# Kernel optimization log

Hardware: AMD Instinct MI355X
Metric: run time of the kernel (lower is better)

## Reference

```python
import jax, jax.numpy as jnp
import numpy as np

B, NUM, LENTH, AUX = 32, 64, 64, 64
SIZE, OUT = 256, 256
IN_G = (LENTH + 1) * 2 + AUX  # 194


def _linear_params(k, fan_in, fan_out):
    # torch nn.Linear default init: U(-1/sqrt(fan_in), 1/sqrt(fan_in))
    s = 1.0 / np.sqrt(fan_in)
    kw, kb = jax.random.split(k)
    W = jax.random.uniform(kw, (fan_in, fan_out), minval=-s, maxval=s, dtype=jnp.float32)
    b = jax.random.uniform(kb, (fan_out,), minval=-s, maxval=s, dtype=jnp.float32)
    return W, b


def setup_inputs() -> dict:
    key = jax.random.key(0)
    ks = jax.random.split(key, 8)
    inp = {"x_aux": jax.random.normal(ks[0], (B, NUM, LENTH + AUX), dtype=jnp.float32)}
    dims = [("g1", IN_G, SIZE), ("g2", SIZE, SIZE), ("g3", SIZE, SIZE), ("g4", SIZE, OUT),
            ("f1", OUT, SIZE), ("f2", SIZE, SIZE), ("f3", SIZE, OUT)]
    for k, (name, fi, fo) in zip(ks[1:], dims):
        W, b = _linear_params(k, fi, fo)
        inp[name + "_w"] = W
        inp[name + "_b"] = b
    return inp


def reference(x_aux, g1_w, g1_b, g2_w, g2_b, g3_w, g3_b, g4_w, g4_b,
              f1_w, f1_b, f2_w, f2_b, f3_w, f3_b):
    bsz = x_aux.shape[0]
    # coord feature = object index i
    coord = jnp.broadcast_to(
        jnp.arange(NUM, dtype=x_aux.dtype)[None, :, None], (bsz, NUM, 1))
    x = jnp.concatenate([x_aux[:, :, :LENTH], coord], axis=-1)      # [B, N, LENTH+1]
    xa = jnp.concatenate([x_aux, coord], axis=-1)                   # [B, N, LENTH+AUX+1]
    # all-pairs broadcast+concat -> [B, N, N, IN_G]
    x_i = jnp.broadcast_to(x[:, None, :, :], (bsz, NUM, NUM, LENTH + 1))
    x_j = jnp.broadcast_to(xa[:, :, None, :], (bsz, NUM, NUM, LENTH + AUX + 1))
    pairs = jnp.concatenate([x_i, x_j], axis=-1)
    # shared g-MLP over every pair
    h = jax.nn.relu(pairs @ g1_w + g1_b)
    h = jax.nn.relu(h @ g2_w + g2_b)
    h = jax.nn.relu(h @ g3_w + g3_b)
    h = jax.nn.relu(h @ g4_w + g4_b)
    # sum-pool over all N*N pairs -> [B, OUT]
    x_g = h.sum(axis=(1, 2))
    # f-MLP (dropout treated as identity / eval mode)
    x_f = jax.nn.relu(x_g @ f1_w + f1_b)
    x_f = jax.nn.relu(x_f @ f2_w + f2_b)
    return x_f @ f3_w + f3_b
```

## Files before the change

### kernel.cpp

```cpp
#include <hip/hip_runtime.h>

#define BATCH 32
#define NOBJ  64
#define PADK  264

typedef _Float16 f16x2 __attribute__((ext_vector_type(2)));
typedef _Float16 f16x4 __attribute__((ext_vector_type(4)));
typedef _Float16 f16x8 __attribute__((ext_vector_type(8)));
typedef float    f32x4 __attribute__((ext_vector_type(4)));
typedef float    f32x16 __attribute__((ext_vector_type(16)));

#define MFMA32(a, b, c) __builtin_amdgcn_mfma_f32_32x32x16_f16((a), (b), (c), 0, 0, 0)


__global__ __launch_bounds__(256) void prep_weights(
    const float* __restrict__ g1w, const float* __restrict__ g2w,
    const float* __restrict__ g3w, const float* __restrict__ g4w,
    _Float16* __restrict__ wtf, float* __restrict__ xg) {
  __shared__ _Float16 tile[256][33];
  const int blk = blockIdx.x;
  const int t = threadIdx.x;
  xg[blk * 256 + t] = 0.0f;

  const int l  = blk >> 3;
  const int nt = blk & 7;
  const float* src = (l == 0) ? g1w : (l == 1) ? g2w : (l == 2) ? g3w : g4w;

  const int nn = t & 31, kb = t >> 5;
#pragma unroll 4
  for (int pass = 0; pass < 32; ++pass) {
    int kp = pass * 8 + kb;
    int kl;
    if (l == 0) {
      if (kp < 64)        kl = kp;
      else if (kp < 192)  kl = kp + 1;
      else if (kp == 192) kl = 64;
      else if (kp == 193) kl = 193;
      else                kl = -1;
    } else {
      kl = 64 * (kp >> 6) + 32 * (kp & 1) + ((kp & 63) >> 1);
    }
    float v = (kl >= 0) ? src[(size_t)kl * 256 + nt * 32 + nn] : 0.0f;
    tile[kp][nn] = (_Float16)v;
  }
  __syncthreads();

  const int lane = t & 63;
  const int nfrag = lane & 31;
  const int kbase = (lane >> 5) * 8;
  _Float16* dst = wtf + ((size_t)(l * 8 + nt) * 16) * 512;
#pragma unroll
  for (int q = 0; q < 4; ++q) {
    int kk = (t >> 6) + 4 * q;
    f16x8 fr;
#pragma unroll
    for (int j = 0; j < 8; ++j)
      fr[j] = tile[kk * 16 + kbase + j][nfrag];
    *(f16x8*)(dst + (size_t)kk * 512 + lane * 8) = fr;
  }
}

template <int STEPS>
__device__ __forceinline__ void do_layer(
    const _Float16* __restrict__ bp0, const _Float16* __restrict__ bp1,
    const _Float16* __restrict__ arow, f32x16 acc[8]) {
  f16x8 b0[STEPS], b1[STEPS];
#pragma unroll
  for (int kk = 0; kk < STEPS; ++kk) {
    b0[kk] = *(const f16x8*)(bp0 + kk * 512);
    b1[kk] = *(const f16x8*)(bp1 + kk * 512);
  }
#pragma unroll
  for (int kk = 0; kk < STEPS; ++kk) {
#pragma unroll
    for (int m = 0; m < 4; ++m) {
      f16x8 a = *(const f16x8*)(arow + (size_t)m * 32 * PADK + kk * 16);
      acc[m * 2]     = MFMA32(a, b0[kk], acc[m * 2]);
      acc[m * 2 + 1] = MFMA32(a, b1[kk], acc[m * 2 + 1]);
    }
  }
}

__global__ __launch_bounds__(256, 2) void g_mlp_pool(
    const float* __restrict__ x_aux,
    const _Float16* __restrict__ wtf,
    const float* __restrict__ g1b, const float* __restrict__ g2b,
    const float* __restrict__ g3b, const float* __restrict__ g4b,
    float* __restrict__ xg) {
  __shared__ _Float16 As[128][PADK];

  const int b  = blockIdx.x >> 5;
  const int i0 = (blockIdx.x & 31) * 2;
  const int t  = threadIdx.x;

  {
    const float* xb = x_aux + (size_t)b * NOBJ * 128;
    {
      const int c4 = t & 15, r0 = t >> 4;
#pragma unroll
      for (int it = 0; it < 8; ++it) {
        int r = it * 16 + r0;
        f32x4 v = *(const f32x4*)(xb + (size_t)(r & 63) * 128 + c4 * 4);
        f16x4 hh = {(_Float16)v[0], (_Float16)v[1], (_Float16)v[2], (_Float16)v[3]};
        *(f16x4*)&As[r][c4 * 4] = hh;
      }
    }
    {
      const int row = t >> 1, seg = t & 1;
      const int ir = i0 + (row >> 6);
      const float* xi = xb + (size_t)ir * 128;
#pragma unroll
      for (int u = 0; u < 8; ++u) {
        int c = seg * 64 + u * 8;
        f32x4 v0 = *(const f32x4*)(xi + c);
        f32x4 v1 = *(const f32x4*)(xi + c + 4);
        f16x8 hh = {(_Float16)v0[0], (_Float16)v0[1], (_Float16)v0[2], (_Float16)v0[3],
                    (_Float16)v1[0], (_Float16)v1[1], (_Float16)v1[2], (_Float16)v1[3]};
        *(f16x8*)&As[row][64 + c] = hh;
      }
      f16x8 z = {};
      *(f16x8*)&As[row][192 + seg * 32]     = z;
      *(f16x8*)&As[row][192 + seg * 32 + 8] = z;
      if (seg == 0) {
        As[row][192] = (_Float16)(row & 63);
        As[row][193] = (_Float16)ir;
      }
    }
  }
  __syncthreads();

  const int lane = t & 63;
  const int nq   = t >> 6;
  const int c31  = lane & 31;
  const int h    = lane >> 5;
  const int n0   = nq * 64;
  const float* gb[4] = {g1b, g2b, g3b, g4b};

  for (int layer = 0; layer < 4; ++layer) {
    const float bv0 = gb[layer][n0 + c31];
    const float bv1 = gb[layer][n0 + 32 + c31];

    f32x16 acc[8] = {};

    const _Float16* bp0 =
        wtf + ((size_t)(layer * 8 + nq * 2) * 16) * 512 + lane * 8;
    const _Float16* bp1 = bp0 + 16 * 512;
    const _Float16* arow = &As[c31][h * 8];

    if (layer == 0)
      do_layer<13>(bp0, bp1, arow, acc);
    else
      do_layer<16>(bp0, bp1, arow, acc);

    if (layer < 3) {
      __syncthreads();
#pragma unroll
      for (int m = 0; m < 4; ++m)
#pragma unroll
        for (int g = 0; g < 4; ++g)
#pragma unroll
          for (int r = 0; r < 4; ++r) {
            const int row = m * 32 + g * 8 + h * 4 + r;
            const int reg = g * 4 + r;
            f16x2 pk = {(_Float16)fmaxf(acc[m * 2][reg] + bv0, 0.f),
                        (_Float16)fmaxf(acc[m * 2 + 1][reg] + bv1, 0.f)};
            *(f16x2*)&As[row][n0 + 2 * c31] = pk;
          }
      __syncthreads();
    } else {
      float s0 = 0.f, s1 = 0.f;
#pragma unroll
      for (int m = 0; m < 4; ++m)
#pragma unroll
        for (int reg = 0; reg < 16; ++reg) {
          s0 += fmaxf(acc[m * 2][reg] + bv0, 0.f);
          s1 += fmaxf(acc[m * 2 + 1][reg] + bv1, 0.f);
        }
      s0 += __shfl_xor(s0, 32, 64);
      s1 += __shfl_xor(s1, 32, 64);
      if (h == 0) {
        atomicAdd(&xg[b * 256 + n0 + c31], s0);
        atomicAdd(&xg[b * 256 + n0 + 32 + c31], s1);
      }
    }
  }
}

__global__ __launch_bounds__(1024) void f_mlp(
    const float* __restrict__ xg,
    const float* __restrict__ f1w, const float* __restrict__ f1b,
    const float* __restrict__ f2w, const float* __restrict__ f2b,
    const float* __restrict__ f3w, const float* __restrict__ f3b,
    float* __restrict__ out) {
  __shared__ float xs[256], ys[256], ps[4][256];
  const int b = blockIdx.x;
  const int t = threadIdx.x;
  const int n = t & 255;
  const int kc = t >> 8;

  if (t < 256) xs[t] = xg[b * 256 + t];
  __syncthreads();

  float p = 0.f;
#pragma unroll 8
  for (int k0 = 0; k0 < 64; ++k0) {
    int k = kc * 64 + k0;
    p += xs[k] * f1w[k * 256 + n];
  }
  ps[kc][n] = p;
  __syncthreads();
  if (t < 256)
    ys[t] = fmaxf(f1b[t] + ps[0][t] + ps[1][t] + ps[2][t] + ps[3][t], 0.f);
  __syncthreads();

  p = 0.f;
#pragma unroll 8
  for (int k0 = 0; k0 < 64; ++k0) {
    int k = kc * 64 + k0;
    p += ys[k] * f2w[k * 256 + n];
  }
  ps[kc][n] = p;
  __syncthreads();
  if (t < 256)
    xs[t] = fmaxf(f2b[t] + ps[0][t] + ps[1][t] + ps[2][t] + ps[3][t], 0.f);
  __syncthreads();

  p = 0.f;
#pragma unroll 8
  for (int k0 = 0; k0 < 64; ++k0) {
    int k = kc * 64 + k0;
    p += xs[k] * f3w[k * 256 + n];
  }
  ps[kc][n] = p;
  __syncthreads();
  if (t < 256)
    out[b * 256 + t] = f3b[t] + ps[0][t] + ps[1][t] + ps[2][t] + ps[3][t];
}

extern "C" void kernel_launch(void* const* d_in, const int* in_sizes, int n_in,
                              void* d_out, int out_size, void* d_ws, size_t ws_size,
                              hipStream_t stream) {
  const float* x_aux = (const float*)d_in[0];
  const float* g1w = (const float*)d_in[1];
  const float* g1b = (const float*)d_in[2];
  const float* g2w = (const float*)d_in[3];
  const float* g2b = (const float*)d_in[4];
  const float* g3w = (const float*)d_in[5];
  const float* g3b = (const float*)d_in[6];
  const float* g4w = (const float*)d_in[7];
  const float* g4b = (const float*)d_in[8];
  const float* f1w = (const float*)d_in[9];
  const float* f1b = (const float*)d_in[10];
  const float* f2w = (const float*)d_in[11];
  const float* f2b = (const float*)d_in[12];
  const float* f3w = (const float*)d_in[13];
  const float* f3b = (const float*)d_in[14];
  float* out = (float*)d_out;

  _Float16* wtf = (_Float16*)d_ws;
  float* xg = (float*)((char*)d_ws + 4u * 256u * 256u * 2u);

  hipLaunchKernelGGL(prep_weights, dim3(32), dim3(256), 0, stream,
                     g1w, g2w, g3w, g4w, wtf, xg);
  hipLaunchKernelGGL(g_mlp_pool, dim3(BATCH * 32), dim3(256), 0, stream,
                     x_aux, wtf, g1b, g2b, g3b, g4b, xg);
  hipLaunchKernelGGL(f_mlp, dim3(BATCH), dim3(1024), 0, stream,
                     xg, f1w, f1b, f2w, f2b, f3w, f3b, out);
}
```

Before: 163.1 us.

## Precompute per-object first-layer contribution to shrink pairwise layer-1 GEMM

Splits the first g-layer matmul into a per-pair part (x_j features plus coord) and a per-object part (the x_i aux features and coord), which is computed once per object in a new kernel. The main kernel initializes its accumulators with this precomputed term and runs only 5 K-steps instead of 13 for layer 1. This cuts redundant MFMA work and the LDS staging of the i-row, at the cost of an extra kernel launch and a global read of the per-object partial sums.

```diff
diff --git a/kernel.cpp b/kernel.cpp
--- a/kernel.cpp
+++ b/kernel.cpp
@@ -12,6 +12,41 @@
 
 #define MFMA32(a, b, c) __builtin_amdgcn_mfma_f32_32x32x16_f16((a), (b), (c), 0, 0, 0)
 
+
+__global__ __launch_bounds__(256) void precompute_ci(
+    const float* __restrict__ x_aux, const float* __restrict__ g1w,
+    float* __restrict__ ci) {
+  __shared__ float xs[4][128];
+  const int blk = blockIdx.x;
+  const int b  = blk >> 4;
+  const int i0 = (blk & 15) * 4;
+  const int t  = threadIdx.x;
+
+#pragma unroll
+  for (int u = 0; u < 2; ++u) {
+    int idx = u * 256 + t;
+    int j = idx >> 7, k = idx & 127;
+    xs[j][k] = x_aux[((size_t)(b * NOBJ + i0 + j)) * 128 + k];
+  }
+  __syncthreads();
+
+  float c0 = 0.f, c1 = 0.f, c2 = 0.f, c3 = 0.f;
+#pragma unroll 8
+  for (int k = 0; k < 128; ++k) {
+    float w = g1w[(size_t)(65 + k) * 256 + t];
+    c0 += xs[0][k] * w; c1 += xs[1][k] * w;
+    c2 += xs[2][k] * w; c3 += xs[3][k] * w;
+  }
+  float wc = g1w[(size_t)193 * 256 + t];
+  c0 += (float)(i0 + 0) * wc;
+  c1 += (float)(i0 + 1) * wc;
+  c2 += (float)(i0 + 2) * wc;
+  c3 += (float)(i0 + 3) * wc;
+  ci[((size_t)(b * NOBJ + i0 + 0)) * 256 + t] = c0;
+  ci[((size_t)(b * NOBJ + i0 + 1)) * 256 + t] = c1;
+  ci[((size_t)(b * NOBJ + i0 + 2)) * 256 + t] = c2;
+  ci[((size_t)(b * NOBJ + i0 + 3)) * 256 + t] = c3;
+}
 
 __global__ __launch_bounds__(256) void prep_weights(
     const float* __restrict__ g1w, const float* __restrict__ g2w,
@@ -32,11 +67,7 @@
     int kp = pass * 8 + kb;
     int kl;
     if (l == 0) {
-      if (kp < 64)        kl = kp;
-      else if (kp < 192)  kl = kp + 1;
-      else if (kp == 192) kl = 64;
-      else if (kp == 193) kl = 193;
-      else                kl = -1;
+      kl = (kp <= 64) ? kp : -1;
     } else {
       kl = 64 * (kp >> 6) + 32 * (kp & 1) + ((kp & 63) >> 1);
     }
@@ -84,6 +115,7 @@
 __global__ __launch_bounds__(256, 2) void g_mlp_pool(
     const float* __restrict__ x_aux,
     const _Float16* __restrict__ wtf,
+    const float* __restrict__ ci,
     const float* __restrict__ g1b, const float* __restrict__ g2b,
     const float* __restrict__ g3b, const float* __restrict__ g4b,
     float* __restrict__ xg) {
@@ -95,36 +127,20 @@
 
   {
     const float* xb = x_aux + (size_t)b * NOBJ * 128;
-    {
-      const int c4 = t & 15, r0 = t >> 4;
-#pragma unroll
-      for (int it = 0; it < 8; ++it) {
-        int r = it * 16 + r0;
-        f32x4 v = *(const f32x4*)(xb + (size_t)(r & 63) * 128 + c4 * 4);
-        f16x4 hh = {(_Float16)v[0], (_Float16)v[1], (_Float16)v[2], (_Float16)v[3]};
-        *(f16x4*)&As[r][c4 * 4] = hh;
-      }
-    }
-    {
-      const int row = t >> 1, seg = t & 1;
-      const int ir = i0 + (row >> 6);
-      const float* xi = xb + (size_t)ir * 128;
-#pragma unroll
-      for (int u = 0; u < 8; ++u) {
-        int c = seg * 64 + u * 8;
-        f32x4 v0 = *(const f32x4*)(xi + c);
-        f32x4 v1 = *(const f32x4*)(xi + c + 4);
-        f16x8 hh = {(_Float16)v0[0], (_Float16)v0[1], (_Float16)v0[2], (_Float16)v0[3],
-                    (_Float16)v1[0], (_Float16)v1[1], (_Float16)v1[2], (_Float16)v1[3]};
-        *(f16x8*)&As[row][64 + c] = hh;
-      }
+    const int c4 = t & 15, r0 = t >> 4;
+#pragma unroll
+    for (int it = 0; it < 8; ++it) {
+      int r = it * 16 + r0;
+      f32x4 v = *(const f32x4*)(xb + (size_t)(r & 63) * 128 + c4 * 4);
+      f16x4 hh = {(_Float16)v[0], (_Float16)v[1], (_Float16)v[2], (_Float16)v[3]};
+      *(f16x4*)&As[r][c4 * 4] = hh;
+    }
+    if (t < 128) {
+      f16x8 z1 = {};
+      z1[0] = (_Float16)(t & 63);
+      *(f16x8*)&As[t][64] = z1;
       f16x8 z = {};
-      *(f16x8*)&As[row][192 + seg * 32]     = z;
-      *(f16x8*)&As[row][192 + seg * 32 + 8] = z;
-      if (seg == 0) {
-        As[row][192] = (_Float16)(row & 63);
-        As[row][193] = (_Float16)ir;
-      }
+      *(f16x8*)&As[t][72] = z;
     }
   }
   __syncthreads();
@@ -136,21 +152,35 @@
   const int n0   = nq * 64;
   const float* gb[4] = {g1b, g2b, g3b, g4b};
 
+  const float* cb = ci + (size_t)(b * NOBJ + i0) * 256;
+  const float ci_v[2][2] = {{cb[n0 + c31], cb[n0 + 32 + c31]},
+                            {cb[256 + n0 + c31], cb[256 + 32 + n0 + c31]}};
+
   for (int layer = 0; layer < 4; ++layer) {
     const float bv0 = gb[layer][n0 + c31];
     const float bv1 = gb[layer][n0 + 32 + c31];
 
-    f32x16 acc[8] = {};
+    f32x16 acc[8];
 
     const _Float16* bp0 =
         wtf + ((size_t)(layer * 8 + nq * 2) * 16) * 512 + lane * 8;
     const _Float16* bp1 = bp0 + 16 * 512;
     const _Float16* arow = &As[c31][h * 8];
 
-    if (layer == 0)
-      do_layer<13>(bp0, bp1, arow, acc);
-    else
+    if (layer == 0) {
+#pragma unroll
+      for (int m = 0; m < 4; ++m)
+#pragma unroll
+        for (int ns = 0; ns < 2; ++ns)
+#pragma unroll
+          for (int reg = 0; reg < 16; ++reg)
+            acc[m * 2 + ns][reg] = ci_v[m >> 1][ns];
+      do_layer<5>(bp0, bp1, arow, acc);
+    } else {
+#pragma unroll
+      for (int x = 0; x < 8; ++x) acc[x] = (f32x16){};
       do_layer<16>(bp0, bp1, arow, acc);
+    }
 
     if (layer < 3) {
       __syncthreads();
@@ -258,12 +288,15 @@
   float* out = (float*)d_out;
 
   _Float16* wtf = (_Float16*)d_ws;
-  float* xg = (float*)((char*)d_ws + 4u * 256u * 256u * 2u);
-
+  float* xg = (float*)((char*)d_ws + 512u * 1024u);
+  float* ci = (float*)((char*)d_ws + 512u * 1024u + 32u * 1024u);
+
+  hipLaunchKernelGGL(precompute_ci, dim3(512), dim3(256), 0, stream,
+                     x_aux, g1w, ci);
   hipLaunchKernelGGL(prep_weights, dim3(32), dim3(256), 0, stream,
                      g1w, g2w, g3w, g4w, wtf, xg);
   hipLaunchKernelGGL(g_mlp_pool, dim3(BATCH * 32), dim3(256), 0, stream,
-                     x_aux, wtf, g1b, g2b, g3b, g4b, xg);
+                     x_aux, wtf, ci, g1b, g2b, g3b, g4b, xg);
   hipLaunchKernelGGL(f_mlp, dim3(BATCH), dim3(1024), 0, stream,
                      xg, f1w, f1b, f2w, f2b, f3w, f3b, out);
 }
```

Measured after the change: 163.3 us. Within noise of the previous version (+0.1%).
